# Kernel tuning notes

Hardware: AMD Instinct MI355X
Metric: run time of the kernel (lower is better)

## Reference

```python
import jax, jax.numpy as jnp
import numpy as np

# dims: T timesteps, B batch, IN input, OUT output, H controller hidden,
# N mem slots, C mem cell size, R read heads
T, B, IN, OUT, H, N, C, R = 512, 64, 256, 256, 512, 2048, 64, 4
EPS = 1e-8


def setup_inputs() -> dict:
    key = jax.random.key(0)
    ks = jax.random.split(key, 12)
    s = 0.02
    d_in = IN + C * R  # controller sees x_t concat flattened read vectors
    return {
        "xs": jax.random.normal(ks[0], (T, B, IN), jnp.float32),
        "W_ih": jax.random.normal(ks[1], (d_in, 4 * H), jnp.float32) * s,
        "W_hh": jax.random.normal(ks[2], (H, 4 * H), jnp.float32) * s,
        "b_lstm": jnp.zeros((4 * H,), jnp.float32),
        "W_out": jax.random.normal(ks[3], (H, OUT), jnp.float32) * s,
        "b_out": jnp.zeros((OUT,), jnp.float32),
        "W_key": jax.random.normal(ks[4], (H, C), jnp.float32) * s,
        "b_key": jnp.zeros((C,), jnp.float32),
        "W_beta": jax.random.normal(ks[5], (H, 1), jnp.float32) * s,
        "b_beta": jnp.zeros((1,), jnp.float32),
        "W_gen": jax.random.normal(ks[6], (H, C), jnp.float32) * s,
        "b_gen": jnp.zeros((C,), jnp.float32),
    }


def reference(xs, W_ih, W_hh, b_lstm, W_out, b_out, W_key, b_key,
              W_beta, b_beta, W_gen, b_gen):
    Bx = xs.shape[1]
    mem0 = jnp.zeros((Bx, N, C), xs.dtype)
    h0 = jnp.zeros((Bx, H), xs.dtype)
    c0 = jnp.zeros((Bx, H), xs.dtype)
    rv0 = jnp.zeros((Bx, C, R), xs.dtype)
    sl0 = jnp.zeros((), xs.dtype)

    def step(carry, x_t):
        h, c, mem, rv, sl = carry
        inp = jnp.concatenate([x_t, rv.reshape(Bx, -1)], axis=-1)
        gates = inp @ W_ih + h @ W_hh + b_lstm
        i_g, f_g, g_g, o_g = jnp.split(gates, 4, axis=-1)
        c = jax.nn.sigmoid(f_g) * c + jax.nn.sigmoid(i_g) * jnp.tanh(g_g)
        h = jax.nn.sigmoid(o_g) * jnp.tanh(c)
        pre_out = h @ W_out + b_out                    # (B, OUT)
        key = h @ W_key + b_key                        # (B, C)
        beta = jax.nn.softplus(h @ W_beta + b_beta)    # (B, 1)
        gen = h @ W_gen + b_gen                        # (B, C)
        # cosine similarity between each memory slot and the key
        num = jnp.einsum('bnc,bc->bn', mem, key)
        den = (jnp.maximum(jnp.linalg.norm(mem, axis=-1), EPS)
               * jnp.maximum(jnp.linalg.norm(key, axis=-1, keepdims=True), EPS))
        sim = num / den                                # (B, N)
        w = jax.nn.softmax(beta * sim, axis=-1)        # (B, N)
        # supervised (teacher) loss for this step
        sl = sl + jnp.mean((key - gen) ** 2)
        # additive content write: rank-1 update
        mem = mem + w[:, :, None] * key[:, None, :]
        # read: weights are the write weights repeated over read heads,
        # so all heads read the same vector -> compute once and broadcast
        r = jnp.einsum('bn,bnc->bc', w, mem)           # (B, C)
        rv = jnp.broadcast_to(r[:, :, None], (Bx, C, R))
        return (h, c, mem, rv, sl), pre_out

    (h, c, mem, rv, sup_loss), y_all = jax.lax.scan(
        step, (h0, c0, mem0, rv0, sl0), xs)
    return y_all, sup_loss
```

## Files before the change

kernel.cpp:

```cpp
#include <hip/hip_runtime.h>
#include <hip/hip_fp16.h>

#define EPSF 1e-8f
#define SCOPE_AGT __HIP_MEMORY_SCOPE_AGENT


typedef _Float16 h2_t __attribute__((ext_vector_type(2)));

struct P5 {
  const unsigned* W2h;
  const float* b_lstm;
  const float* W_out;
  const float* b_out;
  const float* W_key;
  const float* b_key;
  const float* W_beta;
  const float* b_beta;
  const float* W_gen;
  const float* b_gen;
  const float* xs;
  float* hbuf;
  float* AccP;
  float* ZP;
  float* S2P;
  unsigned* ctr;
  float* out;
};

__device__ __forceinline__ float sigm(float x) { return 1.f / (1.f + __expf(-x)); }
__device__ __forceinline__ float aload(const float* p) {
  return __hip_atomic_load(p, __ATOMIC_RELAXED, SCOPE_AGT);
}
__device__ __forceinline__ void astore(float* p, float v) {
  __hip_atomic_store(p, v, __ATOMIC_RELAXED, SCOPE_AGT);
}
__device__ __forceinline__ h2_t u2h(unsigned u) {
  union { unsigned u; h2_t h; } x; x.u = u; return x.h;
}

#if defined(__has_builtin)
#if __has_builtin(__builtin_amdgcn_fdot2)
#define HAVE_FDOT2 1
#endif
#endif

__device__ __forceinline__ float dot2acc(h2_t a, h2_t b, float c) {
#ifdef HAVE_FDOT2
  return __builtin_amdgcn_fdot2(a, b, c, false);
#else
  return fmaf((float)a.x, (float)b.x, fmaf((float)a.y, (float)b.y, c));
#endif
}

__global__ void __launch_bounds__(1024, 4) dnc_b5(P5 P) {
  const int tid   = threadIdx.x;
  const int bid   = blockIdx.x;
  const int chunk = (bid >> 1) & 3;
  const int b     = ((bid >> 3) << 1) | (bid & 1);
  const int lane  = tid & 63;
  const int wv    = tid >> 6;
  const int sgrp  = lane >> 4;
  const int c4    = lane & 15;

  __shared__ _Float16 s_ih[832];
  __shared__ float s_h[512];
  __shared__ float s_gates[512];
  __shared__ float s_c[128];
  __shared__ float s_part[4096];
  __shared__ float s_e[512];
  __shared__ float s_key[64], s_kprev[64], s_genv[64];
  __shared__ float s_wred[32];
  __shared__ float s_scal[4];

  unsigned* ctr = P.ctr + b * 32;

  float4 mreg[8];
  float  sden[8];
#pragma unroll
  for (int i = 0; i < 8; ++i) mreg[i] = make_float4(0.f, 0.f, 0.f, 0.f);

  for (int i = 256 + tid; i < 832; i += 1024) s_ih[i] = (_Float16)0.f;
  if (tid < 512) { s_h[tid] = 0.f; s_e[tid] = 0.f; }
  if (tid < 128) {
    s_c[tid] = 0.f;
    const float2 xv = ((const float2*)P.xs)[(size_t)b * 128 + tid];
    h2_t hv; hv.x = (_Float16)xv.x; hv.y = (_Float16)xv.y;
    *(h2_t*)&s_ih[tid * 2] = hv;
  }
  if (tid < 64) s_kprev[tid] = 0.f;
  float lossacc = 0.f;
  __syncthreads();

  const int q  = tid >> 7;
  const int cg = tid & 127;
  const unsigned* wbase = P.W2h + (size_t)chunk * 212992 + (cg << 2);

  for (int t = 0; t < 512; ++t) {
    float4 acc = make_float4(0.f, 0.f, 0.f, 0.f);
    {
      const unsigned* wp = wbase + (size_t)(q * 48) * 512;
      const _Float16* ip = s_ih + q * 96;
#pragma unroll 4
      for (int r = 0; r < 48; ++r) {
        const uint4 w = *(const uint4*)(wp + (size_t)r * 512);
        const h2_t v = *(const h2_t*)(ip + r * 2);
        acc.x = dot2acc(u2h(w.x), v, acc.x);
        acc.y = dot2acc(u2h(w.y), v, acc.y);
        acc.z = dot2acc(u2h(w.z), v, acc.z);
        acc.w = dot2acc(u2h(w.w), v, acc.w);
      }
    }

    if (t > 0) {
      if (tid == 0) {
        while (__hip_atomic_load(ctr, __ATOMIC_RELAXED, SCOPE_AGT) < 8u * (unsigned)t)
          __builtin_amdgcn_s_sleep(1);
      }
    }
    __syncthreads();
    float a0 = 0.f, a1 = 0.f, a2 = 0.f, a3 = 0.f;
    if (t > 0) {
      if (tid < 64) {
        const float* ap = P.AccP + b * 256 + tid;
        a0 = aload(ap); a1 = aload(ap + 64); a2 = aload(ap + 128); a3 = aload(ap + 192);
      } else if (tid == 64) {
        const float* zp = P.ZP + b * 4;
        const float* sp = P.S2P + b * 4;
        const float Z  = aload(zp) + aload(zp + 1) + aload(zp + 2) + aload(zp + 3);
        const float S2 = aload(sp) + aload(sp + 1) + aload(sp + 2) + aload(sp + 3);
        s_scal[0] = 1.f / Z;  s_scal[1] = S2;
      }
    } else if (tid == 64) {
      s_scal[0] = 0.f; s_scal[1] = 0.f;
    }
    __syncthreads();
    if (t > 0 && tid < 64) {
      const float iZ = s_scal[0];
      const float r = iZ * ((a0 + a1 + a2 + a3) + s_scal[1] * iZ * s_kprev[tid]);
      s_ih[768 + tid] = (_Float16)r;
    }
    __syncthreads();

    {
      const unsigned* wp = wbase + (size_t)(384 + q * 4) * 512;
      const _Float16* ip = s_ih + 768 + q * 8;
#pragma unroll
      for (int r = 0; r < 4; ++r) {
        const uint4 w = *(const uint4*)(wp + (size_t)r * 512);
        const h2_t v = *(const h2_t*)(ip + r * 2);
        acc.x = dot2acc(u2h(w.x), v, acc.x);
        acc.y = dot2acc(u2h(w.y), v, acc.y);
        acc.z = dot2acc(u2h(w.z), v, acc.z);
        acc.w = dot2acc(u2h(w.w), v, acc.w);
      }
    }
    *(float4*)&s_part[(q << 9) + (cg << 2)] = acc;
    __syncthreads();

    if (tid < 512) {
      s_gates[tid] = s_part[tid]        + s_part[512 + tid]  + s_part[1024 + tid] + s_part[1536 + tid]
                   + s_part[2048 + tid] + s_part[2560 + tid] + s_part[3072 + tid] + s_part[3584 + tid];
    }
    __syncthreads();
    if (tid < 128) {
      const int jl = tid, cb = chunk * 128 + jl;
      const float gi = s_gates[jl * 4 + 0] + P.b_lstm[cb];
      const float gf = s_gates[jl * 4 + 1] + P.b_lstm[512 + cb];
      const float gg = s_gates[jl * 4 + 2] + P.b_lstm[1024 + cb];
      const float go = s_gates[jl * 4 + 3] + P.b_lstm[1536 + cb];
      const float cn = sigm(gf) * s_c[jl] + sigm(gi) * tanhf(gg);
      s_c[jl] = cn;
      const float hn = sigm(go) * tanhf(cn);
      s_h[cb] = hn;
      s_ih[256 + cb] = (_Float16)hn;
      astore(P.hbuf + b * 512 + cb, hn);
    }
    __syncthreads();
    if (tid == 0) __hip_atomic_fetch_add(ctr, 1u, __ATOMIC_RELEASE, SCOPE_AGT);

    {
      const float invZp = s_scal[0];
      const float4 kp4 = ((const float4*)s_kprev)[c4];
      const int nbase = (wv * 4 + sgrp) * 8;
#pragma unroll
      for (int it = 0; it < 8; ++it) {
        float4 m4 = mreg[it];
        const float wpv = s_e[nbase + it] * invZp;
        m4.x = fmaf(wpv, kp4.x, m4.x); m4.y = fmaf(wpv, kp4.y, m4.y);
        m4.z = fmaf(wpv, kp4.z, m4.z); m4.w = fmaf(wpv, kp4.w, m4.w);
        float ssq = m4.x * m4.x + m4.y * m4.y + m4.z * m4.z + m4.w * m4.w;
#pragma unroll
        for (int off = 1; off < 16; off <<= 1) ssq += __shfl_xor(ssq, off);
        sden[it] = fmaxf(sqrtf(ssq), EPSF);
        mreg[it] = m4;
      }
    }

    if (tid == 0) {
      while (__hip_atomic_load(ctr, __ATOMIC_RELAXED, SCOPE_AGT) < 8u * (unsigned)t + 4u)
        __builtin_amdgcn_s_sleep(1);
    }
    __syncthreads();
    if (tid < 384) {
      const int pc = tid >> 7;
      const int pcc = pc + (pc >= chunk ? 1 : 0);
      const int jl = tid & 127;
      const float hv = aload(P.hbuf + b * 512 + pcc * 128 + jl);
      s_h[pcc * 128 + jl] = hv;
      s_ih[256 + pcc * 128 + jl] = (_Float16)hv;
    } else if (tid < 512 && t < 511) {
      const int rp = tid - 384;
      const float2 xv = ((const float2*)P.xs)[((size_t)(t + 1) * 64 + b) * 128 + rp];
      h2_t hv; hv.x = (_Float16)xv.x; hv.y = (_Float16)xv.y;
      *(h2_t*)&s_ih[rp * 2] = hv;
    }
    __syncthreads();

    {
      {
        const int rg = tid >> 7, cl = tid & 127;
        const float* W = (cl < 64) ? (P.W_key + cl) : (P.W_gen + (cl - 64));
        const float* hh = s_h + rg * 64;
        float a2 = 0.f;
#pragma unroll 8
        for (int r2 = 0; r2 < 64; ++r2) a2 = fmaf(hh[r2], W[(size_t)(rg * 64 + r2) * 64], a2);
        s_part[rg * 128 + cl] = a2;
      }
      {
        const int rg = tid >> 6, col = tid & 63;
        const float* wp2 = P.W_out + (size_t)(rg * 32) * 256 + chunk * 64 + col;
        const float* hh = s_h + rg * 32;
        float a2 = 0.f;
#pragma unroll 8
        for (int r2 = 0; r2 < 32; ++r2) a2 = fmaf(hh[r2], wp2[(size_t)r2 * 256], a2);
        s_part[1024 + (rg << 6) + col] = a2;
      }
      {
        float pb = (tid < 512) ? s_h[tid] * P.W_beta[tid] : 0.f;
#pragma unroll
        for (int off = 32; off; off >>= 1) pb += __shfl_down(pb, off);
        if (tid < 512 && lane == 0) s_wred[wv] = pb;
      }
    }
    __syncthreads();
    if (tid < 64) {
      float v = 0.f;
#pragma unroll
      for (int k = 0; k < 8; ++k) v += s_part[k * 128 + tid];
      s_key[tid] = v + P.b_key[tid];
    } else if (tid < 128) {
      const int c = tid - 64;
      float v = 0.f;
#pragma unroll
      for (int k = 0; k < 8; ++k) v += s_part[k * 128 + 64 + c];
      s_genv[c] = v + P.b_gen[c];
    } else if (tid < 192) {
      const int col = tid - 128, oc = chunk * 64 + col;
      float v = 0.f;
#pragma unroll
      for (int k = 0; k < 16; ++k) v += s_part[1024 + k * 64 + col];
      P.out[((size_t)t * 64 + b) * 256 + oc] = v + P.b_out[oc];
    } else if (tid == 192) {
      float s = P.b_beta[0];
#pragma unroll
      for (int k = 0; k < 8; ++k) s += s_wred[k];
      s_scal[2] = (s > 20.f) ? s : log1pf(__expf(s));
    }
    __syncthreads();
    if (wv == 0) {
      const float kv = s_key[lane];
      float sq = kv * kv;
#pragma unroll
      for (int off = 32; off; off >>= 1) sq += __shfl_down(sq, off);
      if (lane == 0) s_scal[3] = fmaxf(sqrtf(sq), EPSF);
    } else if (wv == 1 && chunk == 0) {
      const float d = s_key[lane] - s_genv[lane];
      float ds = d * d;
#pragma unroll
      for (int off = 32; off; off >>= 1) ds += __shfl_down(ds, off);
      if (lane == 0) lossacc += ds;
    }
    __syncthreads();

    {
      const float beta = s_scal[2], kn = s_scal[3];
      const float4 kk = ((const float4*)s_key)[c4];
      float Zp = 0.f, S2p = 0.f;
      float4 acc4 = make_float4(0.f, 0.f, 0.f, 0.f);
      const int nbase = (wv * 4 + sgrp) * 8;
#pragma unroll
      for (int it = 0; it < 8; ++it) {
        const float4 m4 = mreg[it];
        float num = m4.x * kk.x + m4.y * kk.y + m4.z * kk.z + m4.w * kk.w;
#pragma unroll
        for (int off = 1; off < 16; off <<= 1) num += __shfl_xor(num, off);
        const float e = __expf(beta * (num / (sden[it] * kn)));
        if (c4 == 0) { s_e[nbase + it] = e; Zp += e; S2p += e * e; }
        acc4.x = fmaf(e, m4.x, acc4.x); acc4.y = fmaf(e, m4.y, acc4.y);
        acc4.z = fmaf(e, m4.z, acc4.z); acc4.w = fmaf(e, m4.w, acc4.w);
      }
#pragma unroll
      for (int off = 32; off; off >>= 1) { Zp += __shfl_down(Zp, off); S2p += __shfl_down(S2p, off); }
      if (lane == 0) { s_wred[wv] = Zp; s_wred[16 + wv] = S2p; }
#pragma unroll
      for (int off = 16; off < 64; off <<= 1) {
        acc4.x += __shfl_down(acc4.x, off); acc4.y += __shfl_down(acc4.y, off);
        acc4.z += __shfl_down(acc4.z, off); acc4.w += __shfl_down(acc4.w, off);
      }
      if (lane < 16) ((float4*)s_part)[wv * 16 + lane] = acc4;
    }
    __syncthreads();
    if (tid < 64) {
      float a = 0.f;
#pragma unroll
      for (int w = 0; w < 16; ++w) a += s_part[w * 64 + tid];
      astore(P.AccP + (b * 4 + chunk) * 64 + tid, a);
      s_kprev[tid] = s_key[tid];
    } else if (tid == 64) {
      float Z = 0.f, S2 = 0.f;
#pragma unroll
      for (int k = 0; k < 16; ++k) { Z += s_wred[k]; S2 += s_wred[16 + k]; }
      astore(P.ZP + b * 4 + chunk, Z);
      astore(P.S2P + b * 4 + chunk, S2);
    }
    __syncthreads();
    if (tid == 0) __hip_atomic_fetch_add(ctr, 1u, __ATOMIC_RELEASE, SCOPE_AGT);
  }

  if (chunk == 0 && tid == 64) atomicAdd(P.out + 8388608, lossacc * (1.f / 4096.f));
}

__global__ void build_w2h(const float* __restrict__ W_ih, const float* __restrict__ W_hh,
                          unsigned* __restrict__ W2h) {
  const int id = blockIdx.x * 256 + threadIdx.x;
  if (id >= 851968) return;
  const int chunk = id / 212992;
  const int rem   = id % 212992;
  const int rp    = rem >> 9;
  const int cc    = rem & 511;
  const int jl = cc >> 2, g = cc & 3;
  const int col = g * 512 + chunk * 128 + jl;
  float v[2];
#pragma unroll
  for (int k = 0; k < 2; ++k) {
    const int row = rp * 2 + k;
    if (row < 256)      v[k] = W_ih[(size_t)row * 2048 + col];
    else if (row < 768) v[k] = W_hh[(size_t)(row - 256) * 2048 + col];
    else {
      const float* p0 = W_ih + (size_t)(256 + (row - 768) * 4) * 2048 + col;
      v[k] = p0[0] + p0[2048] + p0[4096] + p0[6144];
    }
  }
  const __half2 h2v = __floats2half2_rn(v[0], v[1]);
  W2h[id] = *(const unsigned*)&h2v;
}

extern "C" void kernel_launch(void* const* d_in, const int* in_sizes, int n_in,
                              void* d_out, int out_size, void* d_ws, size_t ws_size,
                              hipStream_t stream) {
  const float* xs     = (const float*)d_in[0];
  const float* W_ih   = (const float*)d_in[1];
  const float* W_hh   = (const float*)d_in[2];
  const float* b_lstm = (const float*)d_in[3];
  const float* W_out  = (const float*)d_in[4];
  const float* b_out  = (const float*)d_in[5];
  const float* W_key  = (const float*)d_in[6];
  const float* b_key  = (const float*)d_in[7];
  const float* W_beta = (const float*)d_in[8];
  const float* b_beta = (const float*)d_in[9];
  const float* W_gen  = (const float*)d_in[10];
  const float* b_gen  = (const float*)d_in[11];
  float* out = (float*)d_out;

  float* ws = (float*)d_ws;
  unsigned* W2h = (unsigned*)ws;
  float* hbuf  = ws     + 851968;
  float* AccP  = hbuf   + 32768;
  float* ZP    = AccP   + 16384;
  float* S2P   = ZP     + 256;
  unsigned* ctr = (unsigned*)(S2P + 256);

  hipMemsetAsync(ctr, 0, 2048 * sizeof(unsigned), stream);
  hipMemsetAsync(out + 8388608, 0, sizeof(float), stream);

  build_w2h<<<dim3(3328), dim3(256), 0, stream>>>(W_ih, W_hh, W2h);

  P5 prm;
  prm.W2h = W2h;      prm.b_lstm = b_lstm;
  prm.W_out = W_out;  prm.b_out = b_out;
  prm.W_key = W_key;  prm.b_key = b_key;
  prm.W_beta = W_beta; prm.b_beta = b_beta;
  prm.W_gen = W_gen;  prm.b_gen = b_gen;
  prm.xs = xs;
  prm.hbuf = hbuf; prm.AccP = AccP; prm.ZP = ZP; prm.S2P = S2P;
  prm.ctr = ctr;  prm.out = out;

  void* kargs[] = { &prm };
  hipLaunchCooperativeKernel(reinterpret_cast<void*>(&dnc_b5),
                             dim3(256), dim3(1024), kargs, 0, stream);
}
```

Before: 13.59 ms.

## Repartition LSTM gate GEMM so each block keeps its weight slice in LDS

Before, each block streamed its chunk's fp16 gate weights (about 850KB) from global or L2 on every step. Now each block owns a 3072-word slice of the input and hidden weights resident in LDS, plus the reduced read-vector weights. It computes gate columns for all 64 batches at once, and the partial gates are exchanged through a global buffer with grid-wide counter barriers spread across XCDs. The change also pre-packs x to fp16 ahead of time, stores h in a packed fp16 buffer, and converts the projection weights to fp16. The cost is two extra grid-wide synchronisations per timestep and a dependence on every block being co-resident.

Result: slower. 33.06 ms (+143.3%).

```diff
diff --git a/kernel.cpp b/kernel.cpp
--- a/kernel.cpp
+++ b/kernel.cpp
@@ -7,23 +7,24 @@
 
 typedef _Float16 h2_t __attribute__((ext_vector_type(2)));
 
-struct P5 {
-  const unsigned* W2h;
+struct P6 {
+  const unsigned* W3;
+  const _Float16* Wr;
+  const _Float16* Wp;
   const float* b_lstm;
-  const float* W_out;
   const float* b_out;
-  const float* W_key;
   const float* b_key;
   const float* W_beta;
   const float* b_beta;
-  const float* W_gen;
   const float* b_gen;
-  const float* xs;
-  float* hbuf;
+  const unsigned* xP;
+  unsigned* hP;
+  float* gbuf;
   float* AccP;
   float* ZP;
   float* S2P;
   unsigned* ctr;
+  unsigned* gctr;
   float* out;
 };
 
@@ -34,8 +35,17 @@
 __device__ __forceinline__ void astore(float* p, float v) {
   __hip_atomic_store(p, v, __ATOMIC_RELAXED, SCOPE_AGT);
 }
+__device__ __forceinline__ unsigned aload_u(const unsigned* p) {
+  return __hip_atomic_load(p, __ATOMIC_RELAXED, SCOPE_AGT);
+}
+__device__ __forceinline__ void astore_u(unsigned* p, unsigned v) {
+  __hip_atomic_store(p, v, __ATOMIC_RELAXED, SCOPE_AGT);
+}
 __device__ __forceinline__ h2_t u2h(unsigned u) {
   union { unsigned u; h2_t h; } x; x.u = u; return x.h;
+}
+__device__ __forceinline__ unsigned h2u(h2_t h) {
+  union { h2_t h; unsigned u; } x; x.h = h; return x.u;
 }
 
 #if defined(__has_builtin)
@@ -52,74 +62,89 @@
 #endif
 }
 
-__global__ void __launch_bounds__(1024, 4) dnc_b5(P5 P) {
+__global__ void __launch_bounds__(1024, 4) dnc_b6(P6 P) {
   const int tid   = threadIdx.x;
   const int bid   = blockIdx.x;
-  const int chunk = (bid >> 1) & 3;
-  const int b     = ((bid >> 3) << 1) | (bid & 1);
+  const int chunk = bid & 3;
+  const int b     = bid >> 2;
+  const int qck   = bid >> 6;
+  const int qm    = bid & 63;
   const int lane  = tid & 63;
   const int wv    = tid >> 6;
   const int sgrp  = lane >> 4;
   const int c4    = lane & 15;
-
-  __shared__ _Float16 s_ih[832];
+  const int xcd   = bid & 7;
+
+  __shared__ unsigned  s_w3[3072];
+  __shared__ _Float16  s_wr[32768];
+  __shared__ float s_part[8192];
   __shared__ float s_h[512];
-  __shared__ float s_gates[512];
+  __shared__ float s_gt[512];
+  __shared__ float s_e[512];
+  __shared__ float s_rr[64];
   __shared__ float s_c[128];
-  __shared__ float s_part[4096];
-  __shared__ float s_e[512];
   __shared__ float s_key[64], s_kprev[64], s_genv[64];
   __shared__ float s_wred[32];
   __shared__ float s_scal[4];
 
-  unsigned* ctr = P.ctr + b * 32;
-
   float4 mreg[8];
   float  sden[8];
 #pragma unroll
   for (int i = 0; i < 8; ++i) mreg[i] = make_float4(0.f, 0.f, 0.f, 0.f);
 
-  for (int i = 256 + tid; i < 832; i += 1024) s_ih[i] = (_Float16)0.f;
-  if (tid < 512) { s_h[tid] = 0.f; s_e[tid] = 0.f; }
-  if (tid < 128) {
-    s_c[tid] = 0.f;
-    const float2 xv = ((const float2*)P.xs)[(size_t)b * 128 + tid];
-    h2_t hv; hv.x = (_Float16)xv.x; hv.y = (_Float16)xv.y;
-    *(h2_t*)&s_ih[tid * 2] = hv;
+  for (int i = tid; i < 3072; i += 1024) s_w3[i] = P.W3[(size_t)bid * 3072 + i];
+  {
+    const unsigned* wr32 = (const unsigned*)(P.Wr + (size_t)chunk * 32768);
+    unsigned* swr32 = (unsigned*)s_wr;
+    for (int i = tid; i < 16384; i += 1024) swr32[i] = wr32[i];
   }
-  if (tid < 64) s_kprev[tid] = 0.f;
+  if (tid < 512) s_e[tid] = 0.f;
+  if (tid < 128) s_c[tid] = 0.f;
+  if (tid < 64) { s_kprev[tid] = 0.f; s_rr[tid] = 0.f; }
+  if (tid == 0) { s_scal[0] = 0.f; s_scal[1] = 0.f; s_scal[2] = 0.f; s_scal[3] = 0.f; }
   float lossacc = 0.f;
   __syncthreads();
 
-  const int q  = tid >> 7;
-  const int cg = tid & 127;
-  const unsigned* wbase = P.W2h + (size_t)chunk * 212992 + (cg << 2);
-
   for (int t = 0; t < 512; ++t) {
-    float4 acc = make_float4(0.f, 0.f, 0.f, 0.f);
+    const int par = t & 1;
+
     {
-      const unsigned* wp = wbase + (size_t)(q * 48) * 512;
-      const _Float16* ip = s_ih + q * 96;
-#pragma unroll 4
-      for (int r = 0; r < 48; ++r) {
-        const uint4 w = *(const uint4*)(wp + (size_t)r * 512);
-        const h2_t v = *(const h2_t*)(ip + r * 2);
-        acc.x = dot2acc(u2h(w.x), v, acc.x);
-        acc.y = dot2acc(u2h(w.y), v, acc.y);
-        acc.z = dot2acc(u2h(w.z), v, acc.z);
-        acc.w = dot2acc(u2h(w.w), v, acc.w);
-      }
-    }
+      const unsigned* xrow = P.xP + (size_t)t * 8192;
+      float a8[8] = {0.f, 0.f, 0.f, 0.f, 0.f, 0.f, 0.f, 0.f};
+      const int lo = wv * 24;
+#pragma unroll 8
+      for (int i = 0; i < 24; ++i) {
+        const int rp = lo + i;
+        unsigned uv;
+        if (rp < 128) uv = xrow[rp * 64 + lane];
+        else          uv = aload_u(P.hP + (rp - 128) * 64 + lane);
+        const h2_t vv = u2h(uv);
+        const unsigned* w8 = &s_w3[rp * 8];
+#pragma unroll
+        for (int c = 0; c < 8; ++c) a8[c] = dot2acc(u2h(w8[c]), vv, a8[c]);
+      }
+#pragma unroll
+      for (int c = 0; c < 8; ++c) s_part[(wv * 64 + lane) * 8 + c] = a8[c];
+    }
+    __syncthreads();
+    if (tid < 512) {
+      const int b2 = tid >> 3, c = tid & 7;
+      float v = 0.f;
+#pragma unroll
+      for (int k = 0; k < 16; ++k) v += s_part[(k * 64 + b2) * 8 + c];
+      astore(P.gbuf + par * 131072 + b2 * 2048 + qck * 512 + qm * 8 + c, v);
+    }
+    __syncthreads();
+    if (tid == 0)
+      __hip_atomic_fetch_add(P.gctr + xcd * 32, 1u, __ATOMIC_RELEASE, SCOPE_AGT);
 
     if (t > 0) {
       if (tid == 0) {
-        while (__hip_atomic_load(ctr, __ATOMIC_RELAXED, SCOPE_AGT) < 8u * (unsigned)t)
+        while (__hip_atomic_load(P.ctr + b * 32, __ATOMIC_RELAXED, SCOPE_AGT) < 4u * (unsigned)t)
           __builtin_amdgcn_s_sleep(1);
       }
-    }
-    __syncthreads();
-    float a0 = 0.f, a1 = 0.f, a2 = 0.f, a3 = 0.f;
-    if (t > 0) {
+      __syncthreads();
+      float a0 = 0.f, a1 = 0.f, a2 = 0.f, a3 = 0.f;
       if (tid < 64) {
         const float* ap = P.AccP + b * 256 + tid;
         a0 = aload(ap); a1 = aload(ap + 64); a2 = aload(ap + 128); a3 = aload(ap + 192);
@@ -130,53 +155,60 @@
         const float S2 = aload(sp) + aload(sp + 1) + aload(sp + 2) + aload(sp + 3);
         s_scal[0] = 1.f / Z;  s_scal[1] = S2;
       }
-    } else if (tid == 64) {
-      s_scal[0] = 0.f; s_scal[1] = 0.f;
-    }
-    __syncthreads();
-    if (t > 0 && tid < 64) {
-      const float iZ = s_scal[0];
-      const float r = iZ * ((a0 + a1 + a2 + a3) + s_scal[1] * iZ * s_kprev[tid]);
-      s_ih[768 + tid] = (_Float16)r;
-    }
-    __syncthreads();
-
+      __syncthreads();
+      if (tid < 64) {
+        const float iZ = s_scal[0];
+        s_rr[tid] = iZ * (a0 + a1 + a2 + a3) + s_scal[1] * iZ * iZ * s_kprev[tid];
+      }
+      __syncthreads();
+    }
+
+    if (tid == 0) {
+      const unsigned tgt = 256u * (unsigned)(t + 1);
+      for (;;) {
+        unsigned s = 0;
+#pragma unroll
+        for (int x = 0; x < 8; ++x) s += __hip_atomic_load(P.gctr + x * 32, __ATOMIC_RELAXED, SCOPE_AGT);
+        if (s >= tgt) break;
+        __builtin_amdgcn_s_sleep(1);
+      }
+    }
+    __syncthreads();
     {
-      const unsigned* wp = wbase + (size_t)(384 + q * 4) * 512;
-      const _Float16* ip = s_ih + 768 + q * 8;
-#pragma unroll
-      for (int r = 0; r < 4; ++r) {
-        const uint4 w = *(const uint4*)(wp + (size_t)r * 512);
-        const h2_t v = *(const h2_t*)(ip + r * 2);
-        acc.x = dot2acc(u2h(w.x), v, acc.x);
-        acc.y = dot2acc(u2h(w.y), v, acc.y);
-        acc.z = dot2acc(u2h(w.z), v, acc.z);
-        acc.w = dot2acc(u2h(w.w), v, acc.w);
-      }
-    }
-    *(float4*)&s_part[(q << 9) + (cg << 2)] = acc;
-    __syncthreads();
-
-    if (tid < 512) {
-      s_gates[tid] = s_part[tid]        + s_part[512 + tid]  + s_part[1024 + tid] + s_part[1536 + tid]
-                   + s_part[2048 + tid] + s_part[2560 + tid] + s_part[3072 + tid] + s_part[3584 + tid];
-    }
-    __syncthreads();
+      float gval = 0.f;
+      if (tid < 512) gval = aload(P.gbuf + par * 131072 + b * 2048 + chunk * 512 + tid);
+      const int k = tid & 511, half = tid >> 9;
+      const _Float16* wc = s_wr + half * (32 * 512) + k;
+      const float* rr = s_rr + half * 32;
+      float a = 0.f;
+#pragma unroll 8
+      for (int cI = 0; cI < 32; ++cI) a = fmaf((float)wc[cI * 512], rr[cI], a);
+      s_part[half * 512 + k] = a;
+      if (tid < 512) s_gt[tid] = gval;
+    }
+    __syncthreads();
+
     if (tid < 128) {
-      const int jl = tid, cb = chunk * 128 + jl;
-      const float gi = s_gates[jl * 4 + 0] + P.b_lstm[cb];
-      const float gf = s_gates[jl * 4 + 1] + P.b_lstm[512 + cb];
-      const float gg = s_gates[jl * 4 + 2] + P.b_lstm[1024 + cb];
-      const float go = s_gates[jl * 4 + 3] + P.b_lstm[1536 + cb];
+      const int jl = tid;
+      const int kb = (jl >> 1) * 8 + (jl & 1) * 4;
+      const float gi = s_gt[kb]     + s_part[kb]     + s_part[512 + kb]     + P.b_lstm[chunk * 128 + jl];
+      const float gf = s_gt[kb + 1] + s_part[kb + 1] + s_part[512 + kb + 1] + P.b_lstm[512 + chunk * 128 + jl];
+      const float gg = s_gt[kb + 2] + s_part[kb + 2] + s_part[512 + kb + 2] + P.b_lstm[1024 + chunk * 128 + jl];
+      const float go = s_gt[kb + 3] + s_part[kb + 3] + s_part[512 + kb + 3] + P.b_lstm[1536 + chunk * 128 + jl];
       const float cn = sigm(gf) * s_c[jl] + sigm(gi) * tanhf(gg);
       s_c[jl] = cn;
-      const float hn = sigm(go) * tanhf(cn);
-      s_h[cb] = hn;
-      s_ih[256 + cb] = (_Float16)hn;
-      astore(P.hbuf + b * 512 + cb, hn);
-    }
-    __syncthreads();
-    if (tid == 0) __hip_atomic_fetch_add(ctr, 1u, __ATOMIC_RELEASE, SCOPE_AGT);
+      s_h[chunk * 128 + jl] = sigm(go) * tanhf(cn);
+    }
+    __syncthreads();
+    if (tid < 64) {
+      h2_t hh;
+      hh.x = (_Float16)s_h[chunk * 128 + 2 * tid];
+      hh.y = (_Float16)s_h[chunk * 128 + 2 * tid + 1];
+      astore_u(P.hP + (chunk * 64 + tid) * 64 + b, h2u(hh));
+    }
+    __syncthreads();
+    if (tid == 0)
+      __hip_atomic_fetch_add(P.gctr + 256 + xcd * 32, 1u, __ATOMIC_RELEASE, SCOPE_AGT);
 
     {
       const float invZp = s_scal[0];
@@ -197,43 +229,41 @@
     }
 
     if (tid == 0) {
-      while (__hip_atomic_load(ctr, __ATOMIC_RELAXED, SCOPE_AGT) < 8u * (unsigned)t + 4u)
+      const unsigned tgt = 256u * (unsigned)(t + 1);
+      for (;;) {
+        unsigned s = 0;
+#pragma unroll
+        for (int x = 0; x < 8; ++x) s += __hip_atomic_load(P.gctr + 256 + x * 32, __ATOMIC_RELAXED, SCOPE_AGT);
+        if (s >= tgt) break;
         __builtin_amdgcn_s_sleep(1);
-    }
-    __syncthreads();
-    if (tid < 384) {
-      const int pc = tid >> 7;
-      const int pcc = pc + (pc >= chunk ? 1 : 0);
-      const int jl = tid & 127;
-      const float hv = aload(P.hbuf + b * 512 + pcc * 128 + jl);
-      s_h[pcc * 128 + jl] = hv;
-      s_ih[256 + pcc * 128 + jl] = (_Float16)hv;
-    } else if (tid < 512 && t < 511) {
-      const int rp = tid - 384;
-      const float2 xv = ((const float2*)P.xs)[((size_t)(t + 1) * 64 + b) * 128 + rp];
-      h2_t hv; hv.x = (_Float16)xv.x; hv.y = (_Float16)xv.y;
-      *(h2_t*)&s_ih[rp * 2] = hv;
+      }
+    }
+    __syncthreads();
+    if (tid < 256) {
+      const h2_t hh = u2h(aload_u(P.hP + tid * 64 + b));
+      s_h[2 * tid]     = (float)hh.x;
+      s_h[2 * tid + 1] = (float)hh.y;
     }
     __syncthreads();
 
     {
       {
         const int rg = tid >> 7, cl = tid & 127;
-        const float* W = (cl < 64) ? (P.W_key + cl) : (P.W_gen + (cl - 64));
+        const _Float16* wp = P.Wp + cl;
         const float* hh = s_h + rg * 64;
-        float a2 = 0.f;
+        float a = 0.f;
 #pragma unroll 8
-        for (int r2 = 0; r2 < 64; ++r2) a2 = fmaf(hh[r2], W[(size_t)(rg * 64 + r2) * 64], a2);
-        s_part[rg * 128 + cl] = a2;
+        for (int r = 0; r < 64; ++r) a = fmaf(hh[r], (float)wp[(size_t)(rg * 64 + r) * 384], a);
+        s_part[rg * 128 + cl] = a;
       }
       {
-        const int rg = tid >> 6, col = tid & 63;
-        const float* wp2 = P.W_out + (size_t)(rg * 32) * 256 + chunk * 64 + col;
+        const int rg = tid >> 6, c6 = tid & 63;
+        const _Float16* wp = P.Wp + 128 + chunk * 64 + c6;
         const float* hh = s_h + rg * 32;
-        float a2 = 0.f;
+        float a = 0.f;
 #pragma unroll 8
-        for (int r2 = 0; r2 < 32; ++r2) a2 = fmaf(hh[r2], wp2[(size_t)r2 * 256], a2);
-        s_part[1024 + (rg << 6) + col] = a2;
+        for (int r = 0; r < 32; ++r) a = fmaf(hh[r], (float)wp[(size_t)(rg * 32 + r) * 384], a);
+        s_part[1024 + rg * 64 + c6] = a;
       }
       {
         float pb = (tid < 512) ? s_h[tid] * P.W_beta[tid] : 0.f;
@@ -324,35 +354,62 @@
       astore(P.S2P + b * 4 + chunk, S2);
     }
     __syncthreads();
-    if (tid == 0) __hip_atomic_fetch_add(ctr, 1u, __ATOMIC_RELEASE, SCOPE_AGT);
+    if (tid == 0)
+      __hip_atomic_fetch_add(P.ctr + b * 32, 1u, __ATOMIC_RELEASE, SCOPE_AGT);
   }
 
   if (chunk == 0 && tid == 64) atomicAdd(P.out + 8388608, lossacc * (1.f / 4096.f));
 }
 
-__global__ void build_w2h(const float* __restrict__ W_ih, const float* __restrict__ W_hh,
-                          unsigned* __restrict__ W2h) {
+__global__ void build_w3(const float* __restrict__ W_ih, const float* __restrict__ W_hh,
+                         unsigned* __restrict__ W3) {
   const int id = blockIdx.x * 256 + threadIdx.x;
-  if (id >= 851968) return;
-  const int chunk = id / 212992;
-  const int rem   = id % 212992;
-  const int rp    = rem >> 9;
-  const int cc    = rem & 511;
-  const int jl = cc >> 2, g = cc & 3;
+  if (id >= 786432) return;
+  const int q = id / 3072, rem = id % 3072;
+  const int rp = rem >> 3, c = rem & 7;
+  const int col = (c & 3) * 512 + (q >> 6) * 128 + (q & 63) * 2 + (c >> 2);
+  float v[2];
+#pragma unroll
+  for (int k = 0; k < 2; ++k) {
+    const int row = 2 * rp + k;
+    v[k] = (row < 256) ? W_ih[(size_t)row * 2048 + col]
+                       : W_hh[(size_t)(row - 256) * 2048 + col];
+  }
+  h2_t h; h.x = (_Float16)v[0]; h.y = (_Float16)v[1];
+  W3[id] = h2u(h);
+}
+
+__global__ void build_wr(const float* __restrict__ W_ih, _Float16* __restrict__ Wr) {
+  const int id = blockIdx.x * 256 + threadIdx.x;
+  if (id >= 131072) return;
+  const int chunk = id >> 15, rem = id & 32767;
+  const int cc = rem >> 9, k = rem & 511;
+  const int jl = (k >> 3) * 2 + ((k >> 2) & 1), g = k & 3;
   const int col = g * 512 + chunk * 128 + jl;
-  float v[2];
-#pragma unroll
-  for (int k = 0; k < 2; ++k) {
-    const int row = rp * 2 + k;
-    if (row < 256)      v[k] = W_ih[(size_t)row * 2048 + col];
-    else if (row < 768) v[k] = W_hh[(size_t)(row - 256) * 2048 + col];
-    else {
-      const float* p0 = W_ih + (size_t)(256 + (row - 768) * 4) * 2048 + col;
-      v[k] = p0[0] + p0[2048] + p0[4096] + p0[6144];
-    }
-  }
-  const __half2 h2v = __floats2half2_rn(v[0], v[1]);
-  W2h[id] = *(const unsigned*)&h2v;
+  const float* p0 = W_ih + (size_t)(256 + cc * 4) * 2048 + col;
+  Wr[id] = (_Float16)(p0[0] + p0[2048] + p0[4096] + p0[6144]);
+}
+
+__global__ void build_wp(const float* __restrict__ W_key, const float* __restrict__ W_gen,
+                         const float* __restrict__ W_out, _Float16* __restrict__ Wp) {
+  const int id = blockIdx.x * 256 + threadIdx.x;
+  if (id >= 196608) return;
+  const int row = id / 384, cl = id % 384;
+  float v;
+  if (cl < 64)       v = W_key[(size_t)row * 64 + cl];
+  else if (cl < 128) v = W_gen[(size_t)row * 64 + cl - 64];
+  else               v = W_out[(size_t)row * 256 + cl - 128];
+  Wp[id] = (_Float16)v;
+}
+
+__global__ void build_xp(const float* __restrict__ xs, unsigned* __restrict__ xP) {
+  const int id = blockIdx.x * 256 + threadIdx.x;
+  if (id >= 4194304) return;
+  const int t = id >> 13, rem = id & 8191;
+  const int rp = rem >> 6, bb = rem & 63;
+  const float* p = xs + ((size_t)t * 64 + bb) * 256 + 2 * rp;
+  h2_t h; h.x = (_Float16)p[0]; h.y = (_Float16)p[1];
+  xP[id] = h2u(h);
 }
 
 extern "C" void kernel_launch(void* const* d_in, const int* in_sizes, int n_in,
@@ -373,29 +430,36 @@
   float* out = (float*)d_out;
 
   float* ws = (float*)d_ws;
-  unsigned* W2h = (unsigned*)ws;
-  float* hbuf  = ws     + 851968;
-  float* AccP  = hbuf   + 32768;
-  float* ZP    = AccP   + 16384;
-  float* S2P   = ZP     + 256;
-  unsigned* ctr = (unsigned*)(S2P + 256);
-
-  hipMemsetAsync(ctr, 0, 2048 * sizeof(unsigned), stream);
+  unsigned*  W3  = (unsigned*)ws;
+  _Float16*  Wr  = (_Float16*)(ws + 786432);
+  _Float16*  Wp  = (_Float16*)(ws + 851968);
+  unsigned*  xP  = (unsigned*)(ws + 950272);
+  unsigned*  hP  = (unsigned*)(ws + 5144576);
+  float*     gbuf = ws + 5160960;
+  float*     AccP = ws + 5423104;
+  float*     ZP   = ws + 5439488;
+  float*     S2P  = ws + 5439744;
+  unsigned*  ctr  = (unsigned*)(ws + 5440000);
+  unsigned*  gctr = (unsigned*)(ws + 5442048);
+
+  hipMemsetAsync(hP, 0, 16384 * sizeof(unsigned), stream);
+  hipMemsetAsync(ctr, 0, (2048 + 512) * sizeof(unsigned), stream);
   hipMemsetAsync(out + 8388608, 0, sizeof(float), stream);
 
-  build_w2h<<<dim3(3328), dim3(256), 0, stream>>>(W_ih, W_hh, W2h);
-
-  P5 prm;
-  prm.W2h = W2h;      prm.b_lstm = b_lstm;
-  prm.W_out = W_out;  prm.b_out = b_out;
-  prm.W_key = W_key;  prm.b_key = b_key;
-  prm.W_beta = W_beta; prm.b_beta = b_beta;
-  prm.W_gen = W_gen;  prm.b_gen = b_gen;
-  prm.xs = xs;
-  prm.hbuf = hbuf; prm.AccP = AccP; prm.ZP = ZP; prm.S2P = S2P;
-  prm.ctr = ctr;  prm.out = out;
+  build_w3<<<dim3(3072),  dim3(256), 0, stream>>>(W_ih, W_hh, W3);
+  build_wr<<<dim3(512),   dim3(256), 0, stream>>>(W_ih, Wr);
+  build_wp<<<dim3(768),   dim3(256), 0, stream>>>(W_key, W_gen, W_out, Wp);
+  build_xp<<<dim3(16384), dim3(256), 0, stream>>>(xs, xP);
+
+  P6 prm;
+  prm.W3 = W3; prm.Wr = Wr; prm.Wp = Wp;
+  prm.b_lstm = b_lstm; prm.b_out = b_out; prm.b_key = b_key;
+  prm.W_beta = W_beta; prm.b_beta = b_beta; prm.b_gen = b_gen;
+  prm.xP = xP; prm.hP = hP; prm.gbuf = gbuf;
+  prm.AccP = AccP; prm.ZP = ZP; prm.S2P = S2P;
+  prm.ctr = ctr; prm.gctr = gctr; prm.out = out;
 
   void* kargs[] = { &prm };
-  hipLaunchCooperativeKernel(reinterpret_cast<void*>(&dnc_b5),
+  hipLaunchCooperativeKernel(reinterpret_cast<void*>(&dnc_b6),
                              dim3(256), dim3(1024), kargs, 0, stream);
 }
```

## Split each batch row across eight 512-thread blocks with fp16 head weights

Applied to the files above, without the earlier changes.

Each batch element's work is now split over 8 blocks of 512 threads instead of 4 blocks of 1024, which halves the per-block share of gate columns and memory slots. The packed LSTM weight layout, the cross-block reductions and the counter barriers are resized to match. The key/gen and output projection weights are pre-converted to fp16 to cut load bandwidth. The cooperative launch is replaced by a regular launch with dynamic shared memory, so spin-wait barriers now rely on all 512 blocks being co-resident. More blocks per batch element also means more inter-block synchronization per step.

Measured after the change: 19.66 ms. 44.7% more time.

```diff
diff --git a/kernel.cpp b/kernel.cpp
--- a/kernel.cpp
+++ b/kernel.cpp
@@ -7,16 +7,15 @@
 
 typedef _Float16 h2_t __attribute__((ext_vector_type(2)));
 
-struct P5 {
+struct P8 {
   const unsigned* W2h;
+  const _Float16* Wkg;
+  const _Float16* Wy;
   const float* b_lstm;
-  const float* W_out;
   const float* b_out;
-  const float* W_key;
   const float* b_key;
   const float* W_beta;
   const float* b_beta;
-  const float* W_gen;
   const float* b_gen;
   const float* xs;
   float* hbuf;
@@ -52,11 +51,11 @@
 #endif
 }
 
-__global__ void __launch_bounds__(1024, 4) dnc_b5(P5 P) {
+__global__ void __launch_bounds__(512, 4) dnc_b8(P8 P) {
   const int tid   = threadIdx.x;
   const int bid   = blockIdx.x;
-  const int chunk = (bid >> 1) & 3;
-  const int b     = ((bid >> 3) << 1) | (bid & 1);
+  const int chunk = bid & 7;
+  const int b     = bid >> 3;
   const int lane  = tid & 63;
   const int wv    = tid >> 6;
   const int sgrp  = lane >> 4;
@@ -64,45 +63,47 @@
 
   __shared__ _Float16 s_ih[832];
   __shared__ float s_h[512];
-  __shared__ float s_gates[512];
-  __shared__ float s_c[128];
-  __shared__ float s_part[4096];
-  __shared__ float s_e[512];
+  __shared__ float s_gates[256];
+  __shared__ float s_c[64];
+  __shared__ float s_part[2048];
+  __shared__ float s_e[256];
   __shared__ float s_key[64], s_kprev[64], s_genv[64];
   __shared__ float s_wred[32];
+  __shared__ float s_bred[8];
   __shared__ float s_scal[4];
 
-  unsigned* ctr = P.ctr + b * 32;
+  unsigned* ctr = P.ctr + b * 16;
 
   float4 mreg[8];
   float  sden[8];
 #pragma unroll
   for (int i = 0; i < 8; ++i) mreg[i] = make_float4(0.f, 0.f, 0.f, 0.f);
 
-  for (int i = 256 + tid; i < 832; i += 1024) s_ih[i] = (_Float16)0.f;
-  if (tid < 512) { s_h[tid] = 0.f; s_e[tid] = 0.f; }
+  for (int i = 256 + tid; i < 832; i += 512) s_ih[i] = (_Float16)0.f;
+  if (tid < 512) s_h[tid] = 0.f;
+  if (tid < 256) s_e[tid] = 0.f;
+  if (tid < 64) { s_c[tid] = 0.f; s_kprev[tid] = 0.f; }
   if (tid < 128) {
-    s_c[tid] = 0.f;
     const float2 xv = ((const float2*)P.xs)[(size_t)b * 128 + tid];
     h2_t hv; hv.x = (_Float16)xv.x; hv.y = (_Float16)xv.y;
     *(h2_t*)&s_ih[tid * 2] = hv;
   }
-  if (tid < 64) s_kprev[tid] = 0.f;
+  if (tid == 0) { s_scal[0] = 0.f; s_scal[1] = 0.f; }
   float lossacc = 0.f;
   __syncthreads();
 
-  const int q  = tid >> 7;
-  const int cg = tid & 127;
-  const unsigned* wbase = P.W2h + (size_t)chunk * 212992 + (cg << 2);
+  const int q  = tid >> 6;
+  const int cg = tid & 63;
+  const unsigned* wbase = P.W2h + (size_t)chunk * 106496 + (cg << 2);
 
   for (int t = 0; t < 512; ++t) {
     float4 acc = make_float4(0.f, 0.f, 0.f, 0.f);
     {
-      const unsigned* wp = wbase + (size_t)(q * 48) * 512;
+      const unsigned* wp = wbase + (size_t)(q * 48) * 256;
       const _Float16* ip = s_ih + q * 96;
 #pragma unroll 4
       for (int r = 0; r < 48; ++r) {
-        const uint4 w = *(const uint4*)(wp + (size_t)r * 512);
+        const uint4 w = *(const uint4*)(wp + (size_t)r * 256);
         const h2_t v = *(const h2_t*)(ip + r * 2);
         acc.x = dot2acc(u2h(w.x), v, acc.x);
         acc.y = dot2acc(u2h(w.y), v, acc.y);
@@ -113,40 +114,40 @@
 
     if (t > 0) {
       if (tid == 0) {
-        while (__hip_atomic_load(ctr, __ATOMIC_RELAXED, SCOPE_AGT) < 8u * (unsigned)t)
+        while (__hip_atomic_load(ctr, __ATOMIC_RELAXED, SCOPE_AGT) < 16u * (unsigned)t)
           __builtin_amdgcn_s_sleep(1);
       }
     }
     __syncthreads();
-    float a0 = 0.f, a1 = 0.f, a2 = 0.f, a3 = 0.f;
+    float a0 = 0.f;
     if (t > 0) {
       if (tid < 64) {
-        const float* ap = P.AccP + b * 256 + tid;
-        a0 = aload(ap); a1 = aload(ap + 64); a2 = aload(ap + 128); a3 = aload(ap + 192);
+        const float* ap = P.AccP + b * 512 + tid;
+#pragma unroll
+        for (int k = 0; k < 8; ++k) a0 += aload(ap + k * 64);
       } else if (tid == 64) {
-        const float* zp = P.ZP + b * 4;
-        const float* sp = P.S2P + b * 4;
-        const float Z  = aload(zp) + aload(zp + 1) + aload(zp + 2) + aload(zp + 3);
-        const float S2 = aload(sp) + aload(sp + 1) + aload(sp + 2) + aload(sp + 3);
+        const float* zp = P.ZP + b * 8;
+        const float* sp = P.S2P + b * 8;
+        float Z = 0.f, S2 = 0.f;
+#pragma unroll
+        for (int k = 0; k < 8; ++k) { Z += aload(zp + k); S2 += aload(sp + k); }
         s_scal[0] = 1.f / Z;  s_scal[1] = S2;
       }
-    } else if (tid == 64) {
-      s_scal[0] = 0.f; s_scal[1] = 0.f;
     }
     __syncthreads();
     if (t > 0 && tid < 64) {
       const float iZ = s_scal[0];
-      const float r = iZ * ((a0 + a1 + a2 + a3) + s_scal[1] * iZ * s_kprev[tid]);
+      const float r = iZ * a0 + s_scal[1] * iZ * iZ * s_kprev[tid];
       s_ih[768 + tid] = (_Float16)r;
     }
     __syncthreads();
 
     {
-      const unsigned* wp = wbase + (size_t)(384 + q * 4) * 512;
+      const unsigned* wp = wbase + (size_t)(384 + q * 4) * 256;
       const _Float16* ip = s_ih + 768 + q * 8;
 #pragma unroll
       for (int r = 0; r < 4; ++r) {
-        const uint4 w = *(const uint4*)(wp + (size_t)r * 512);
+        const uint4 w = *(const uint4*)(wp + (size_t)r * 256);
         const h2_t v = *(const h2_t*)(ip + r * 2);
         acc.x = dot2acc(u2h(w.x), v, acc.x);
         acc.y = dot2acc(u2h(w.y), v, acc.y);
@@ -154,16 +155,18 @@
         acc.w = dot2acc(u2h(w.w), v, acc.w);
       }
     }
-    *(float4*)&s_part[(q << 9) + (cg << 2)] = acc;
-    __syncthreads();
-
-    if (tid < 512) {
-      s_gates[tid] = s_part[tid]        + s_part[512 + tid]  + s_part[1024 + tid] + s_part[1536 + tid]
-                   + s_part[2048 + tid] + s_part[2560 + tid] + s_part[3072 + tid] + s_part[3584 + tid];
-    }
-    __syncthreads();
-    if (tid < 128) {
-      const int jl = tid, cb = chunk * 128 + jl;
+    *(float4*)&s_part[(q << 8) + (cg << 2)] = acc;
+    __syncthreads();
+
+    if (tid < 256) {
+      float g = 0.f;
+#pragma unroll
+      for (int k = 0; k < 8; ++k) g += s_part[(k << 8) + tid];
+      s_gates[tid] = g;
+    }
+    __syncthreads();
+    if (tid < 64) {
+      const int jl = tid, cb = chunk * 64 + jl;
       const float gi = s_gates[jl * 4 + 0] + P.b_lstm[cb];
       const float gf = s_gates[jl * 4 + 1] + P.b_lstm[512 + cb];
       const float gg = s_gates[jl * 4 + 2] + P.b_lstm[1024 + cb];
@@ -197,73 +200,77 @@
     }
 
     if (tid == 0) {
-      while (__hip_atomic_load(ctr, __ATOMIC_RELAXED, SCOPE_AGT) < 8u * (unsigned)t + 4u)
+      while (__hip_atomic_load(ctr, __ATOMIC_RELAXED, SCOPE_AGT) < 16u * (unsigned)t + 8u)
         __builtin_amdgcn_s_sleep(1);
     }
     __syncthreads();
-    if (tid < 384) {
-      const int pc = tid >> 7;
+    if (tid < 448) {
+      const int pc = tid >> 6;
       const int pcc = pc + (pc >= chunk ? 1 : 0);
-      const int jl = tid & 127;
-      const float hv = aload(P.hbuf + b * 512 + pcc * 128 + jl);
-      s_h[pcc * 128 + jl] = hv;
-      s_ih[256 + pcc * 128 + jl] = (_Float16)hv;
-    } else if (tid < 512 && t < 511) {
-      const int rp = tid - 384;
-      const float2 xv = ((const float2*)P.xs)[((size_t)(t + 1) * 64 + b) * 128 + rp];
-      h2_t hv; hv.x = (_Float16)xv.x; hv.y = (_Float16)xv.y;
-      *(h2_t*)&s_ih[rp * 2] = hv;
+      const int jl = tid & 63;
+      const float hv = aload(P.hbuf + b * 512 + pcc * 64 + jl);
+      s_h[pcc * 64 + jl] = hv;
+      s_ih[256 + pcc * 64 + jl] = (_Float16)hv;
+    } else if (t < 511) {
+      const int i2 = tid - 448;
+#pragma unroll
+      for (int k = 0; k < 2; ++k) {
+        const int rp = i2 * 2 + k;
+        const float2 xv = ((const float2*)P.xs)[((size_t)(t + 1) * 64 + b) * 128 + rp];
+        h2_t hv; hv.x = (_Float16)xv.x; hv.y = (_Float16)xv.y;
+        *(h2_t*)&s_ih[rp * 2] = hv;
+      }
     }
     __syncthreads();
 
     {
       {
         const int rg = tid >> 7, cl = tid & 127;
-        const float* W = (cl < 64) ? (P.W_key + cl) : (P.W_gen + (cl - 64));
-        const float* hh = s_h + rg * 64;
-        float a2 = 0.f;
+        const _Float16* wp = P.Wkg + cl;
+        const float* hh = s_h + rg * 128;
+        float a = 0.f;
 #pragma unroll 8
-        for (int r2 = 0; r2 < 64; ++r2) a2 = fmaf(hh[r2], W[(size_t)(rg * 64 + r2) * 64], a2);
-        s_part[rg * 128 + cl] = a2;
+        for (int r = 0; r < 128; ++r) a = fmaf(hh[r], (float)wp[(size_t)(rg * 128 + r) * 128], a);
+        s_part[rg * 128 + cl] = a;
       }
       {
-        const int rg = tid >> 6, col = tid & 63;
-        const float* wp2 = P.W_out + (size_t)(rg * 32) * 256 + chunk * 64 + col;
+        const int rg = tid >> 5, c5 = tid & 31;
+        const _Float16* wp = P.Wy + chunk * 32 + c5;
         const float* hh = s_h + rg * 32;
-        float a2 = 0.f;
+        float a = 0.f;
 #pragma unroll 8
-        for (int r2 = 0; r2 < 32; ++r2) a2 = fmaf(hh[r2], wp2[(size_t)r2 * 256], a2);
-        s_part[1024 + (rg << 6) + col] = a2;
+        for (int r = 0; r < 32; ++r) a = fmaf(hh[r], (float)wp[(size_t)(rg * 32 + r) * 256], a);
+        s_part[1024 + (rg << 5) + c5] = a;
       }
       {
-        float pb = (tid < 512) ? s_h[tid] * P.W_beta[tid] : 0.f;
+        float pb = s_h[tid] * P.W_beta[tid];
 #pragma unroll
         for (int off = 32; off; off >>= 1) pb += __shfl_down(pb, off);
-        if (tid < 512 && lane == 0) s_wred[wv] = pb;
+        if (lane == 0) s_bred[wv] = pb;
       }
     }
     __syncthreads();
     if (tid < 64) {
       float v = 0.f;
 #pragma unroll
-      for (int k = 0; k < 8; ++k) v += s_part[k * 128 + tid];
+      for (int k = 0; k < 4; ++k) v += s_part[k * 128 + tid];
       s_key[tid] = v + P.b_key[tid];
     } else if (tid < 128) {
       const int c = tid - 64;
       float v = 0.f;
 #pragma unroll
-      for (int k = 0; k < 8; ++k) v += s_part[k * 128 + 64 + c];
+      for (int k = 0; k < 4; ++k) v += s_part[k * 128 + 64 + c];
       s_genv[c] = v + P.b_gen[c];
-    } else if (tid < 192) {
-      const int col = tid - 128, oc = chunk * 64 + col;
+    } else if (tid < 160) {
+      const int col = tid - 128, oc = chunk * 32 + col;
       float v = 0.f;
 #pragma unroll
-      for (int k = 0; k < 16; ++k) v += s_part[1024 + k * 64 + col];
+      for (int k = 0; k < 16; ++k) v += s_part[1024 + (k << 5) + col];
       P.out[((size_t)t * 64 + b) * 256 + oc] = v + P.b_out[oc];
-    } else if (tid == 192) {
+    } else if (tid == 160) {
       float s = P.b_beta[0];
 #pragma unroll
-      for (int k = 0; k < 8; ++k) s += s_wred[k];
+      for (int k = 0; k < 8; ++k) s += s_bred[k];
       s_scal[2] = (s > 20.f) ? s : log1pf(__expf(s));
     }
     __syncthreads();
@@ -313,15 +320,15 @@
     if (tid < 64) {
       float a = 0.f;
 #pragma unroll
-      for (int w = 0; w < 16; ++w) a += s_part[w * 64 + tid];
-      astore(P.AccP + (b * 4 + chunk) * 64 + tid, a);
+      for (int w = 0; w < 8; ++w) a += s_part[w * 64 + tid];
+      astore(P.AccP + (b * 8 + chunk) * 64 + tid, a);
       s_kprev[tid] = s_key[tid];
     } else if (tid == 64) {
       float Z = 0.f, S2 = 0.f;
 #pragma unroll
-      for (int k = 0; k < 16; ++k) { Z += s_wred[k]; S2 += s_wred[16 + k]; }
-      astore(P.ZP + b * 4 + chunk, Z);
-      astore(P.S2P + b * 4 + chunk, S2);
+      for (int k = 0; k < 8; ++k) { Z += s_wred[k]; S2 += s_wred[16 + k]; }
+      astore(P.ZP + b * 8 + chunk, Z);
+      astore(P.S2P + b * 8 + chunk, S2);
     }
     __syncthreads();
     if (tid == 0) __hip_atomic_fetch_add(ctr, 1u, __ATOMIC_RELEASE, SCOPE_AGT);
@@ -330,16 +337,16 @@
   if (chunk == 0 && tid == 64) atomicAdd(P.out + 8388608, lossacc * (1.f / 4096.f));
 }
 
-__global__ void build_w2h(const float* __restrict__ W_ih, const float* __restrict__ W_hh,
-                          unsigned* __restrict__ W2h) {
+__global__ void build_w2h8(const float* __restrict__ W_ih, const float* __restrict__ W_hh,
+                           unsigned* __restrict__ W2h) {
   const int id = blockIdx.x * 256 + threadIdx.x;
   if (id >= 851968) return;
-  const int chunk = id / 212992;
-  const int rem   = id % 212992;
-  const int rp    = rem >> 9;
-  const int cc    = rem & 511;
+  const int chunk = id / 106496;
+  const int rem   = id % 106496;
+  const int rp    = rem >> 8;
+  const int cc    = rem & 255;
   const int jl = cc >> 2, g = cc & 3;
-  const int col = g * 512 + chunk * 128 + jl;
+  const int col = g * 512 + chunk * 64 + jl;
   float v[2];
 #pragma unroll
   for (int k = 0; k < 2; ++k) {
@@ -353,6 +360,21 @@
   }
   const __half2 h2v = __floats2half2_rn(v[0], v[1]);
   W2h[id] = *(const unsigned*)&h2v;
+}
+
+__global__ void build_wkg(const float* __restrict__ W_key, const float* __restrict__ W_gen,
+                          _Float16* __restrict__ Wkg) {
+  const int id = blockIdx.x * 256 + threadIdx.x;
+  if (id >= 65536) return;
+  const int row = id >> 7, cl = id & 127;
+  const float v = (cl < 64) ? W_key[(size_t)row * 64 + cl] : W_gen[(size_t)row * 64 + cl - 64];
+  Wkg[id] = (_Float16)v;
+}
+
+__global__ void build_wy(const float* __restrict__ W_out, _Float16* __restrict__ Wy) {
+  const int id = blockIdx.x * 256 + threadIdx.x;
+  if (id >= 131072) return;
+  Wy[id] = (_Float16)W_out[id];
 }
 
 extern "C" void kernel_launch(void* const* d_in, const int* in_sizes, int n_in,
@@ -374,28 +396,28 @@
 
   float* ws = (float*)d_ws;
   unsigned* W2h = (unsigned*)ws;
-  float* hbuf  = ws     + 851968;
-  float* AccP  = hbuf   + 32768;
-  float* ZP    = AccP   + 16384;
-  float* S2P   = ZP     + 256;
-  unsigned* ctr = (unsigned*)(S2P + 256);
-
-  hipMemsetAsync(ctr, 0, 2048 * sizeof(unsigned), stream);
+  _Float16* Wkg = (_Float16*)(ws + 851968);
+  _Float16* Wy  = (_Float16*)(ws + 884736);
+  float* hbuf  = ws + 950272;
+  float* AccP  = hbuf + 32768;
+  float* ZP    = AccP + 32768;
+  float* S2P   = ZP + 512;
+  unsigned* ctr = (unsigned*)(S2P + 512);
+
+  hipMemsetAsync(ctr, 0, 1024 * sizeof(unsigned), stream);
   hipMemsetAsync(out + 8388608, 0, sizeof(float), stream);
 
-  build_w2h<<<dim3(3328), dim3(256), 0, stream>>>(W_ih, W_hh, W2h);
-
-  P5 prm;
-  prm.W2h = W2h;      prm.b_lstm = b_lstm;
-  prm.W_out = W_out;  prm.b_out = b_out;
-  prm.W_key = W_key;  prm.b_key = b_key;
-  prm.W_beta = W_beta; prm.b_beta = b_beta;
-  prm.W_gen = W_gen;  prm.b_gen = b_gen;
+  build_w2h8<<<dim3(3328), dim3(256), 0, stream>>>(W_ih, W_hh, W2h);
+  build_wkg<<<dim3(256),  dim3(256), 0, stream>>>(W_key, W_gen, Wkg);
+  build_wy<<<dim3(512),   dim3(256), 0, stream>>>(W_out, Wy);
+
+  P8 prm;
+  prm.W2h = W2h; prm.Wkg = Wkg; prm.Wy = Wy;
+  prm.b_lstm = b_lstm; prm.b_out = b_out; prm.b_key = b_key;
+  prm.W_beta = W_beta; prm.b_beta = b_beta; prm.b_gen = b_gen;
   prm.xs = xs;
   prm.hbuf = hbuf; prm.AccP = AccP; prm.ZP = ZP; prm.S2P = S2P;
-  prm.ctr = ctr;  prm.out = out;
-
-  void* kargs[] = { &prm };
-  hipLaunchCooperativeKernel(reinterpret_cast<void*>(&dnc_b5),
-                             dim3(256), dim3(1024), kargs, 0, stream);
-}
+  prm.ctr = ctr; prm.out = out;
+
+  dnc_b8<<<dim3(512), dim3(512), 40960, stream>>>(prm);
+}
```
